# Kernel optimization log

Measured on AMD Instinct MI355X. Metric: run time of the kernel, lower is better.

Reference implementation:

```python
import jax, jax.numpy as jnp
import numpy as np

N_NODES = 100000
N_EDGES = 1600000
F_IN, F_HID, F_OUT = 15, 64, 64
N_MID = 6  # layers 1..6 of 8


def gcn_norm(edge_index, edge_weight, num_nodes):
    """PyG GCNConv normalization with self-loops (fill_value=1.0).
    Returns (src, dst, norm) over the augmented edge set."""
    src, dst = edge_index[0], edge_index[1]
    loop = jnp.arange(num_nodes)
    s = jnp.concatenate([src, loop])
    d = jnp.concatenate([dst, loop])
    w = jnp.concatenate([edge_weight, jnp.ones((num_nodes,), edge_weight.dtype)])
    deg = jax.ops.segment_sum(w, d, num_segments=num_nodes)
    dinv = jnp.where(deg > 0, jax.lax.rsqrt(deg), 0.0)
    norm = dinv[s] * w * dinv[d]  # [E+N]
    return s, d, norm


def gcn_layer(h, s, d, norm, W, b, num_nodes):
    h = h @ W                                  # dense transform [N, F_out]
    msg = norm[:, None] * h[s]                 # gather + scale   [E+N, F_out]
    out = jax.ops.segment_sum(msg, d, num_segments=num_nodes)  # scatter-add
    return out + b


def setup_inputs() -> dict:
    key = jax.random.key(0)
    ks = jax.random.split(key, 8)
    x = jax.random.normal(ks[0], (N_NODES, F_IN), jnp.float32)
    edge_index = jax.random.randint(ks[1], (2, N_EDGES), 0, N_NODES, jnp.int64)
    edge_weight = jax.random.uniform(ks[2], (N_EDGES,), jnp.float32)
    # glorot-ish scaling keeps activations sane through 8 layers
    W0 = jax.random.normal(ks[3], (F_IN, F_HID), jnp.float32) * (1.0 / np.sqrt(F_IN))
    b0 = jnp.zeros((F_HID,), jnp.float32)
    W_mid = jax.random.normal(ks[4], (N_MID, F_HID, F_HID), jnp.float32) * (1.0 / np.sqrt(F_HID))
    b_mid = jnp.zeros((N_MID, F_HID), jnp.float32)
    W_last = jax.random.normal(ks[5], (F_HID, F_OUT), jnp.float32) * (1.0 / np.sqrt(F_HID))
    b_last = jnp.zeros((F_OUT,), jnp.float32)
    return {"x": x, "edge_index": edge_index, "edge_weight": edge_weight,
            "W0": W0, "b0": b0, "W_mid": W_mid, "b_mid": b_mid,
            "W_last": W_last, "b_last": b_last}


def reference(x, edge_index, edge_weight, W0, b0, W_mid, b_mid, W_last, b_last):
    num_nodes = x.shape[0]
    s, d, norm = gcn_norm(edge_index, edge_weight, num_nodes)
    # layer 0
    h = gcn_layer(x, s, d, norm, W0, b0, num_nodes)
    h = jax.nn.relu(h)  # dropout is identity in eval mode
    # middle layers 1..6
    for i in range(N_MID):
        h = gcn_layer(h, s, d, norm, W_mid[i], b_mid[i], num_nodes)
        h = jax.nn.relu(h)
    # final layer + sigmoid
    h = gcn_layer(h, s, d, norm, W_last, b_last, num_nodes)
    return jax.nn.sigmoid(h)
```

## Files before the change

### kernel.cpp

```cpp
#include <hip/hip_runtime.h>
#include <hip/hip_fp16.h>
#include <math.h>

#define N_NODES 100000
#define N_EDGES 1600000
#define F_IN 15
#define MASK40 ((1ull << 40) - 1)

#define NBLK1 256
#define EPB   (N_EDGES / NBLK1)
#define NBUCK 256
#define NBUCK_USED ((N_NODES + 511) >> 9)

typedef _Float16 half8 __attribute__((ext_vector_type(8)));
typedef float f32x4 __attribute__((ext_vector_type(4)));


__global__ __launch_bounds__(1024) void k_hist(const int* __restrict__ dst,
                                               int* __restrict__ hist) {
    __shared__ int bins[NBUCK];
    int t = threadIdx.x, blk = blockIdx.x;
    if (t < NBUCK) bins[t] = 0;
    __syncthreads();
    int e0 = blk * EPB;
    for (int e = e0 + t; e < e0 + EPB; e += 1024)
        atomicAdd(&bins[dst[e] >> 9], 1);
    __syncthreads();
    if (t < NBUCK) hist[t * NBLK1 + blk] = bins[t];
}

__global__ __launch_bounds__(1024) void k_scan(int* __restrict__ hist,
                                               int* __restrict__ bucketBase,
                                               int* __restrict__ rowptr) {
    __shared__ int sc[1024];
    int t = threadIdx.x;
    int base = t * 64;
    int vals[64];
    int tot = 0;
#pragma unroll
    for (int k = 0; k < 64; k++) { vals[k] = hist[base + k]; tot += vals[k]; }
    sc[t] = tot;
    __syncthreads();
    for (int off = 1; off < 1024; off <<= 1) {
        int u = (t >= off) ? sc[t - off] : 0;
        __syncthreads();
        sc[t] += u;
        __syncthreads();
    }
    int run = sc[t] - tot;
#pragma unroll
    for (int k = 0; k < 64; k++) {
        int idx = base + k;
        if ((idx & (NBLK1 - 1)) == 0) bucketBase[idx / NBLK1] = run;
        int v = vals[k];
        hist[idx] = run;
        run += v;
    }
    if (t == 0) { bucketBase[NBUCK] = N_EDGES; rowptr[N_NODES] = N_EDGES; }
}

__global__ __launch_bounds__(1024) void k_scatter(const int* __restrict__ src,
        const int* __restrict__ dst, const float* __restrict__ w,
        const int* __restrict__ hist, int2* __restrict__ brec) {
    __shared__ int cursor[NBUCK];
    int t = threadIdx.x, blk = blockIdx.x;
    if (t < NBUCK) cursor[t] = hist[t * NBLK1 + blk];
    __syncthreads();
    int e0 = blk * EPB;
    for (int e = e0 + t; e < e0 + EPB; e += 1024) {
        int d = dst[e];
        int pos = atomicAdd(&cursor[d >> 9], 1);
        brec[pos] = make_int2(src[e] | ((d & 511) << 17), __float_as_int(w[e]));
    }
}

__global__ __launch_bounds__(512) void k_deg(const int2* __restrict__ brec,
        const int* __restrict__ bucketBase, float* __restrict__ dinv,
        int* __restrict__ rowptr) {
    __shared__ unsigned long long packedl[512];
    __shared__ int sc[512];
    int t = threadIdx.x, b = blockIdx.x;
    packedl[t] = 0ull;
    __syncthreads();
    int ebase = bucketBase[b], eend = bucketBase[b + 1];
    for (int e = ebase + t; e < eend; e += 512) {
        int2 r = brec[e];
        int dlo = (r.x >> 17) & 511;
        float wv = __int_as_float(r.y);
        unsigned long long contrib =
            (1ull << 40) + (unsigned long long)((double)wv * 4294967296.0);
        atomicAdd(&packedl[dlo], contrib);
    }
    __syncthreads();
    unsigned long long p = packedl[t];
    int cnt = (int)(p >> 40);
    int n = (b << 9) + t;
    if (n < N_NODES) {
        float deg = 1.0f + (float)((double)(p & MASK40) * 0x1p-32);
        dinv[n] = rsqrtf(deg);
    }
    sc[t] = cnt;
    __syncthreads();
    for (int off = 1; off < 512; off <<= 1) {
        int u = (t >= off) ? sc[t - off] : 0;
        __syncthreads();
        sc[t] += u;
        __syncthreads();
    }
    if (n < N_NODES) rowptr[n] = ebase + sc[t] - cnt;
}

__global__ __launch_bounds__(512) void k_csr(const int2* __restrict__ brec,
        const int* __restrict__ bucketBase, const int* __restrict__ rowptr,
        const float* __restrict__ dinv, int2* __restrict__ csr) {
    __shared__ int cursor[512];
    __shared__ float dl[512];
    int t = threadIdx.x, b = blockIdx.x;
    int n = (b << 9) + t;
    if (n < N_NODES) { cursor[t] = rowptr[n]; dl[t] = dinv[n]; }
    else             { cursor[t] = 0;         dl[t] = 0.f; }
    __syncthreads();
    int ebase = bucketBase[b], eend = bucketBase[b + 1];
    for (int e = ebase + t; e < eend; e += 512) {
        int2 r = brec[e];
        int dlo = (r.x >> 17) & 511;
        int s = r.x & 0x1FFFF;
        float wv = __int_as_float(r.y);
        int slot = atomicAdd(&cursor[dlo], 1);
        float nm = dinv[s] * wv * dl[dlo];
        csr[slot] = make_int2(s << 7, __float_as_int(nm));
    }
}


__global__ void k_gemm0(const float* __restrict__ x, const float* __restrict__ W,
                        __half* __restrict__ out) {
    __shared__ float Ws[F_IN * 64];
    int t = threadIdx.x;
    for (int i = t; i < F_IN * 64; i += 256) Ws[i] = W[i];
    __syncthreads();
    int r = blockIdx.x * 4 + (t >> 6);
    int c = t & 63;
    if (r < N_NODES) {
        const float* xr = x + r * F_IN;
        float acc = 0.f;
#pragma unroll
        for (int k = 0; k < F_IN; k++) acc += xr[k] * Ws[k * 64 + c];
        out[r * 64 + c] = __float2half(acc);
    }
}


#define SE_CAP 128
#define G_STRIDE 72

template <bool WEP, bool SIG>
__global__ __launch_bounds__(256, 8) void k_gather4(
        const int* __restrict__ rowptr, const int2* __restrict__ csr,
        const __half* __restrict__ hin, const float* __restrict__ dinv,
        const float* __restrict__ W, const float* __restrict__ b,
        void* __restrict__ outp) {
    extern __shared__ char smem[];
    int t = threadIdx.x, wv = t >> 6, lane = t & 63;
    int sub = lane >> 5, fl = lane & 31;
    int2* se = (int2*)smem + wv * SE_CAP;
    _Float16* G = (_Float16*)(smem + 4 * SE_CAP * 8);

    int nb = blockIdx.x * 32;
    int n0w = nb + wv * 8;

    int rp[9];
#pragma unroll
    for (int j = 0; j < 9; j++) rp[j] = rowptr[n0w + j];
    int base = rp[0], end = rp[8];

    const char* hb = (const char*)hin;
    unsigned flb = (unsigned)fl * 4u;

    const __half2* h2 = (const __half2*)hin;
    float2 acc[8];
#pragma unroll
    for (int j = 0; j < 8; j++) {
        int n = n0w + j;
        float dv = dinv[n];
        __half2 hq = h2[n * 32 + fl];
        float w0 = (sub == 0) ? dv * dv : 0.f;
        acc[j].x = w0 * __low2float(hq);
        acc[j].y = w0 * __high2float(hq);
    }

    for (int cb = base; cb < end; cb += SE_CAP) {
        int ce = cb + SE_CAP; if (ce > end) ce = end;
        int cn = ce - cb;
        for (int i = lane; i < cn; i += 64) se[i] = csr[cb + i];
        __builtin_amdgcn_wave_barrier();
#pragma unroll
        for (int j = 0; j < 8; j++) {
            int lo = rp[j] < cb ? cb : rp[j];
            int hi = rp[j + 1] > ce ? ce : rp[j + 1];
            int i = lo - cb, iend = hi - cb;
            for (; i + 7 < iend; i += 8) {
                int2 r0 = se[i + sub],     r1 = se[i + 2 + sub];
                int2 r2 = se[i + 4 + sub], r3 = se[i + 6 + sub];
                __half2 q0 = *(const __half2*)(hb + (size_t)((unsigned)r0.x + flb));
                __half2 q1 = *(const __half2*)(hb + (size_t)((unsigned)r1.x + flb));
                __half2 q2 = *(const __half2*)(hb + (size_t)((unsigned)r2.x + flb));
                __half2 q3 = *(const __half2*)(hb + (size_t)((unsigned)r3.x + flb));
                float n0 = __int_as_float(r0.y), n1 = __int_as_float(r1.y);
                float n2 = __int_as_float(r2.y), n3 = __int_as_float(r3.y);
                acc[j].x = fmaf(n0, __low2float(q0), acc[j].x);
                acc[j].y = fmaf(n0, __high2float(q0), acc[j].y);
                acc[j].x = fmaf(n1, __low2float(q1), acc[j].x);
                acc[j].y = fmaf(n1, __high2float(q1), acc[j].y);
                acc[j].x = fmaf(n2, __low2float(q2), acc[j].x);
                acc[j].y = fmaf(n2, __high2float(q2), acc[j].y);
                acc[j].x = fmaf(n3, __low2float(q3), acc[j].x);
                acc[j].y = fmaf(n3, __high2float(q3), acc[j].y);
            }
            for (; i + 1 < iend; i += 2) {
                int2 r = se[i + sub];
                __half2 q = *(const __half2*)(hb + (size_t)((unsigned)r.x + flb));
                float nm = __int_as_float(r.y);
                acc[j].x = fmaf(nm, __low2float(q), acc[j].x);
                acc[j].y = fmaf(nm, __high2float(q), acc[j].y);
            }
            if (i < iend) {
                int2 r = se[i];
                __half2 q = *(const __half2*)(hb + (size_t)((unsigned)r.x + flb));
                float nm = (sub == 0) ? __int_as_float(r.y) : 0.f;
                acc[j].x = fmaf(nm, __low2float(q), acc[j].x);
                acc[j].y = fmaf(nm, __high2float(q), acc[j].y);
            }
        }
        __builtin_amdgcn_wave_barrier();
    }

#pragma unroll
    for (int j = 0; j < 8; j++) {
        acc[j].x += __shfl_xor(acc[j].x, 32);
        acc[j].y += __shfl_xor(acc[j].y, 32);
    }

    if (!WEP) {
        float2 bv = ((const float2*)b)[fl];
        if (sub == 0) {
#pragma unroll
            for (int j = 0; j < 8; j++) {
                float ox = fmaxf(acc[j].x + bv.x, 0.f);
                float oy = fmaxf(acc[j].y + bv.y, 0.f);
                ((__half2*)outp)[(n0w + j) * 32 + fl] = __floats2half2_rn(ox, oy);
            }
        }
        return;
    }

    if (sub == 0) {
        __half2* G2 = (__half2*)G;
#pragma unroll
        for (int j = 0; j < 8; j++)
            G2[(wv * 8 + j) * (G_STRIDE / 2) + fl] = __floats2half2_rn(acc[j].x, acc[j].y);
    }
    __syncthreads();

    int col = lane & 15, quad = lane >> 4;
    int mrow = (wv & 1) * 16;
    int nc0 = (wv >> 1) * 32;

    half8 af[2];
#pragma unroll
    for (int kt = 0; kt < 2; kt++)
        af[kt] = *(const half8*)&G[(mrow + col) * G_STRIDE + kt * 32 + quad * 8];

    __syncthreads();

    half8 bf[2][2][2];
#pragma unroll
    for (int nt = 0; nt < 2; nt++) {
#pragma unroll
        for (int kt = 0; kt < 2; kt++) {
#pragma unroll
            for (int j = 0; j < 8; j++) {
                float w = W[(kt * 32 + quad * 8 + j) * 64 + nc0 + nt * 16 + col];
                _Float16 hi = (_Float16)w;
                bf[nt][kt][0][j] = hi;
                bf[nt][kt][1][j] = (_Float16)(w - (float)hi);
            }
        }
    }

    f32x4 c0, c1;
    {
        float b0v = b[nc0 + col], b1v = b[nc0 + 16 + col];
        c0 = (f32x4){b0v, b0v, b0v, b0v};
        c1 = (f32x4){b1v, b1v, b1v, b1v};
    }
#pragma unroll
    for (int kt = 0; kt < 2; kt++) {
        c0 = __builtin_amdgcn_mfma_f32_16x16x32_f16(af[kt], bf[0][kt][0], c0, 0, 0, 0);
        c0 = __builtin_amdgcn_mfma_f32_16x16x32_f16(af[kt], bf[0][kt][1], c0, 0, 0, 0);
        c1 = __builtin_amdgcn_mfma_f32_16x16x32_f16(af[kt], bf[1][kt][0], c1, 0, 0, 0);
        c1 = __builtin_amdgcn_mfma_f32_16x16x32_f16(af[kt], bf[1][kt][1], c1, 0, 0, 0);
    }

    if (!SIG) {
#pragma unroll
        for (int nt = 0; nt < 2; nt++) {
            f32x4 c = nt ? c1 : c0;
#pragma unroll
            for (int r = 0; r < 4; r++) {
                float o = fmaxf(c[r], 0.f);
                G[(mrow + quad * 4 + r) * G_STRIDE + nc0 + nt * 16 + col] =
                    (_Float16)o;
            }
        }
        __syncthreads();
        {
            int row = t >> 3, seg = t & 7;
            half8 v = *(const half8*)&G[row * G_STRIDE + seg * 8];
            *(half8*)((__half*)outp + (nb + row) * 64 + seg * 8) = v;
        }
    } else {
        float* fo = (float*)smem;
#pragma unroll
        for (int nt = 0; nt < 2; nt++) {
            f32x4 c = nt ? c1 : c0;
#pragma unroll
            for (int r = 0; r < 4; r++) {
                float o = 1.0f / (1.0f + expf(-c[r]));
                fo[(mrow + quad * 4 + r) * 66 + nc0 + nt * 16 + col] = o;
            }
        }
        __syncthreads();
#pragma unroll
        for (int k = 0; k < 2; k++) {
            int lin = t + k * 256;
            int row = lin >> 4, seg = lin & 15;
            float4 v = *(const float4*)&fo[row * 66 + seg * 4];
            *(float4*)((float*)outp + (nb + row) * 64 + seg * 4) = v;
        }
    }
}


extern "C" void kernel_launch(void* const* d_in, const int* in_sizes, int n_in,
                              void* d_out, int out_size, void* d_ws, size_t ws_size,
                              hipStream_t stream) {
    const float* x  = (const float*)d_in[0];
    const int*   ei = (const int*)  d_in[1];
    const float* ew = (const float*)d_in[2];
    const float* W0 = (const float*)d_in[3];
    const float* b0 = (const float*)d_in[4];
    const float* Wm = (const float*)d_in[5];
    const float* bm = (const float*)d_in[6];
    const float* Wl = (const float*)d_in[7];
    const float* bl = (const float*)d_in[8];
    float* out = (float*)d_out;

    const int* src = ei;
    const int* dst = ei + N_EDGES;

    char* ws = (char*)d_ws;
    int*    hist   = (int*)  (ws + 0);
    int*    bbase  = (int*)  (ws + (1u << 18));
    float*  dinv   = (float*)(ws + (1u << 20));
    int*    rowptr = (int*)  (ws + (2u << 20));
    int2*   brec   = (int2*) (ws + (3u << 20));
    int2*   csr    = (int2*) (ws + (16u << 20));
    __half* htmp   = (__half*)(ws + (29u << 20));
    __half* hA     = (__half*)(ws + (42u << 20));
    __half* hB     = (__half*)(ws + (55u << 20));

    int gR4 = (N_NODES + 3) / 4;
    int gG  = N_NODES / 32;

    const size_t smem0 = 4 * SE_CAP * 8;
    const size_t smemW = 4 * SE_CAP * 8 + 32 * G_STRIDE * 2;

    hipLaunchKernelGGL(k_hist,    dim3(NBLK1), dim3(1024), 0, stream, dst, hist);
    hipLaunchKernelGGL(k_scan,    dim3(1),     dim3(1024), 0, stream, hist, bbase, rowptr);
    hipLaunchKernelGGL(k_scatter, dim3(NBLK1), dim3(1024), 0, stream, src, dst, ew, hist, brec);
    hipLaunchKernelGGL(k_deg,     dim3(NBUCK_USED), dim3(512), 0, stream, brec, bbase, dinv, rowptr);
    hipLaunchKernelGGL(k_csr,     dim3(NBUCK_USED), dim3(512), 0, stream, brec, bbase, rowptr, dinv, csr);

    hipLaunchKernelGGL(k_gemm0,   dim3(gR4), dim3(256), 0, stream, x, W0, htmp);
    hipLaunchKernelGGL((k_gather4<false, false>), dim3(gG), dim3(256), smem0, stream,
                       rowptr, csr, htmp, dinv, (const float*)nullptr, b0, (void*)hA);

    __half* hin = hA;
    __half* hout = hB;
    for (int i = 0; i < 6; i++) {
        const float* Wi = Wm + (long)i * 64 * 64;
        const float* bi = bm + (long)i * 64;
        hipLaunchKernelGGL((k_gather4<true, false>), dim3(gG), dim3(256), smemW, stream,
                           rowptr, csr, hin, dinv, Wi, bi, (void*)hout);
        __half* t2 = hin; hin = hout; hout = t2;
    }

    hipLaunchKernelGGL((k_gather4<true, true>), dim3(gG), dim3(256), smemW, stream,
                       rowptr, csr, hin, dinv, Wl, bl, (void*)out);
}
```

Measured before the change: 506.0 us.

## Make gather kernels persistent with atomic tile queue for dynamic load balancing

The per-layer gather kernels now launch a fixed grid of 2048 blocks. Each block repeatedly takes the next 32-node tile from a global atomic counter until all 3125 tiles are done. The counters are zeroed in the scan kernel, one per layer. This aims to balance the uneven per-tile edge counts and cut block scheduling overhead, at the cost of an atomic and extra block-wide barriers per tile.

```diff
diff --git a/kernel.cpp b/kernel.cpp
--- a/kernel.cpp
+++ b/kernel.cpp
@@ -11,6 +11,9 @@
 #define EPB   (N_EDGES / NBLK1)
 #define NBUCK 256
 #define NBUCK_USED ((N_NODES + 511) >> 9)
+
+#define NT_TILES 3125
+#define PERSIST_BLOCKS 2048
 
 typedef _Float16 half8 __attribute__((ext_vector_type(8)));
 typedef float f32x4 __attribute__((ext_vector_type(4)));
@@ -31,7 +34,8 @@
 
 __global__ __launch_bounds__(1024) void k_scan(int* __restrict__ hist,
                                                int* __restrict__ bucketBase,
-                                               int* __restrict__ rowptr) {
+                                               int* __restrict__ rowptr,
+                                               int* __restrict__ tick) {
     __shared__ int sc[1024];
     int t = threadIdx.x;
     int base = t * 64;
@@ -57,6 +61,7 @@
         run += v;
     }
     if (t == 0) { bucketBase[NBUCK] = N_EDGES; rowptr[N_NODES] = N_EDGES; }
+    if (t < 8) tick[t] = 0;
 }
 
 __global__ __launch_bounds__(1024) void k_scatter(const int* __restrict__ src,
@@ -159,185 +164,195 @@
         const int* __restrict__ rowptr, const int2* __restrict__ csr,
         const __half* __restrict__ hin, const float* __restrict__ dinv,
         const float* __restrict__ W, const float* __restrict__ b,
-        void* __restrict__ outp) {
+        int* __restrict__ tick, void* __restrict__ outp) {
     extern __shared__ char smem[];
+    __shared__ int s_tile;
     int t = threadIdx.x, wv = t >> 6, lane = t & 63;
     int sub = lane >> 5, fl = lane & 31;
     int2* se = (int2*)smem + wv * SE_CAP;
     _Float16* G = (_Float16*)(smem + 4 * SE_CAP * 8);
 
-    int nb = blockIdx.x * 32;
-    int n0w = nb + wv * 8;
-
-    int rp[9];
-#pragma unroll
-    for (int j = 0; j < 9; j++) rp[j] = rowptr[n0w + j];
-    int base = rp[0], end = rp[8];
-
     const char* hb = (const char*)hin;
     unsigned flb = (unsigned)fl * 4u;
-
     const __half2* h2 = (const __half2*)hin;
-    float2 acc[8];
-#pragma unroll
-    for (int j = 0; j < 8; j++) {
-        int n = n0w + j;
-        float dv = dinv[n];
-        __half2 hq = h2[n * 32 + fl];
-        float w0 = (sub == 0) ? dv * dv : 0.f;
-        acc[j].x = w0 * __low2float(hq);
-        acc[j].y = w0 * __high2float(hq);
-    }
-
-    for (int cb = base; cb < end; cb += SE_CAP) {
-        int ce = cb + SE_CAP; if (ce > end) ce = end;
-        int cn = ce - cb;
-        for (int i = lane; i < cn; i += 64) se[i] = csr[cb + i];
-        __builtin_amdgcn_wave_barrier();
+
+    for (;;) {
+        if (t == 0) s_tile = atomicAdd(tick, 1);
+        __syncthreads();
+        int tile = s_tile;
+        if (tile >= NT_TILES) break;
+
+        int nb = tile * 32;
+        int n0w = nb + wv * 8;
+
+        int rp[9];
+#pragma unroll
+        for (int j = 0; j < 9; j++) rp[j] = rowptr[n0w + j];
+        int base = rp[0], end = rp[8];
+
+        float2 acc[8];
 #pragma unroll
         for (int j = 0; j < 8; j++) {
-            int lo = rp[j] < cb ? cb : rp[j];
-            int hi = rp[j + 1] > ce ? ce : rp[j + 1];
-            int i = lo - cb, iend = hi - cb;
-            for (; i + 7 < iend; i += 8) {
-                int2 r0 = se[i + sub],     r1 = se[i + 2 + sub];
-                int2 r2 = se[i + 4 + sub], r3 = se[i + 6 + sub];
-                __half2 q0 = *(const __half2*)(hb + (size_t)((unsigned)r0.x + flb));
-                __half2 q1 = *(const __half2*)(hb + (size_t)((unsigned)r1.x + flb));
-                __half2 q2 = *(const __half2*)(hb + (size_t)((unsigned)r2.x + flb));
-                __half2 q3 = *(const __half2*)(hb + (size_t)((unsigned)r3.x + flb));
-                float n0 = __int_as_float(r0.y), n1 = __int_as_float(r1.y);
-                float n2 = __int_as_float(r2.y), n3 = __int_as_float(r3.y);
-                acc[j].x = fmaf(n0, __low2float(q0), acc[j].x);
-                acc[j].y = fmaf(n0, __high2float(q0), acc[j].y);
-                acc[j].x = fmaf(n1, __low2float(q1), acc[j].x);
-                acc[j].y = fmaf(n1, __high2float(q1), acc[j].y);
-                acc[j].x = fmaf(n2, __low2float(q2), acc[j].x);
-                acc[j].y = fmaf(n2, __high2float(q2), acc[j].y);
-                acc[j].x = fmaf(n3, __low2float(q3), acc[j].x);
-                acc[j].y = fmaf(n3, __high2float(q3), acc[j].y);
-            }
-            for (; i + 1 < iend; i += 2) {
-                int2 r = se[i + sub];
-                __half2 q = *(const __half2*)(hb + (size_t)((unsigned)r.x + flb));
-                float nm = __int_as_float(r.y);
-                acc[j].x = fmaf(nm, __low2float(q), acc[j].x);
-                acc[j].y = fmaf(nm, __high2float(q), acc[j].y);
-            }
-            if (i < iend) {
-                int2 r = se[i];
-                __half2 q = *(const __half2*)(hb + (size_t)((unsigned)r.x + flb));
-                float nm = (sub == 0) ? __int_as_float(r.y) : 0.f;
-                acc[j].x = fmaf(nm, __low2float(q), acc[j].x);
-                acc[j].y = fmaf(nm, __high2float(q), acc[j].y);
-            }
-        }
-        __builtin_amdgcn_wave_barrier();
-    }
-
-#pragma unroll
-    for (int j = 0; j < 8; j++) {
-        acc[j].x += __shfl_xor(acc[j].x, 32);
-        acc[j].y += __shfl_xor(acc[j].y, 32);
-    }
-
-    if (!WEP) {
-        float2 bv = ((const float2*)b)[fl];
+            int n = n0w + j;
+            float dv = dinv[n];
+            __half2 hq = h2[n * 32 + fl];
+            float w0 = (sub == 0) ? dv * dv : 0.f;
+            acc[j].x = w0 * __low2float(hq);
+            acc[j].y = w0 * __high2float(hq);
+        }
+
+        for (int cb = base; cb < end; cb += SE_CAP) {
+            int ce = cb + SE_CAP; if (ce > end) ce = end;
+            int cn = ce - cb;
+            for (int i = lane; i < cn; i += 64) se[i] = csr[cb + i];
+            __builtin_amdgcn_wave_barrier();
+#pragma unroll
+            for (int j = 0; j < 8; j++) {
+                int lo = rp[j] < cb ? cb : rp[j];
+                int hi = rp[j + 1] > ce ? ce : rp[j + 1];
+                int i = lo - cb, iend = hi - cb;
+                for (; i + 7 < iend; i += 8) {
+                    int2 r0 = se[i + sub],     r1 = se[i + 2 + sub];
+                    int2 r2 = se[i + 4 + sub], r3 = se[i + 6 + sub];
+                    __half2 q0 = *(const __half2*)(hb + (size_t)((unsigned)r0.x + flb));
+                    __half2 q1 = *(const __half2*)(hb + (size_t)((unsigned)r1.x + flb));
+                    __half2 q2 = *(const __half2*)(hb + (size_t)((unsigned)r2.x + flb));
+                    __half2 q3 = *(const __half2*)(hb + (size_t)((unsigned)r3.x + flb));
+                    float n0 = __int_as_float(r0.y), n1 = __int_as_float(r1.y);
+                    float n2 = __int_as_float(r2.y), n3 = __int_as_float(r3.y);
+                    acc[j].x = fmaf(n0, __low2float(q0), acc[j].x);
+                    acc[j].y = fmaf(n0, __high2float(q0), acc[j].y);
+                    acc[j].x = fmaf(n1, __low2float(q1), acc[j].x);
+                    acc[j].y = fmaf(n1, __high2float(q1), acc[j].y);
+                    acc[j].x = fmaf(n2, __low2float(q2), acc[j].x);
+                    acc[j].y = fmaf(n2, __high2float(q2), acc[j].y);
+                    acc[j].x = fmaf(n3, __low2float(q3), acc[j].x);
+                    acc[j].y = fmaf(n3, __high2float(q3), acc[j].y);
+                }
+                for (; i + 1 < iend; i += 2) {
+                    int2 r = se[i + sub];
+                    __half2 q = *(const __half2*)(hb + (size_t)((unsigned)r.x + flb));
+                    float nm = __int_as_float(r.y);
+                    acc[j].x = fmaf(nm, __low2float(q), acc[j].x);
+                    acc[j].y = fmaf(nm, __high2float(q), acc[j].y);
+                }
+                if (i < iend) {
+                    int2 r = se[i];
+                    __half2 q = *(const __half2*)(hb + (size_t)((unsigned)r.x + flb));
+                    float nm = (sub == 0) ? __int_as_float(r.y) : 0.f;
+                    acc[j].x = fmaf(nm, __low2float(q), acc[j].x);
+                    acc[j].y = fmaf(nm, __high2float(q), acc[j].y);
+                }
+            }
+            __builtin_amdgcn_wave_barrier();
+        }
+
+#pragma unroll
+        for (int j = 0; j < 8; j++) {
+            acc[j].x += __shfl_xor(acc[j].x, 32);
+            acc[j].y += __shfl_xor(acc[j].y, 32);
+        }
+
+        if (!WEP) {
+            float2 bv = ((const float2*)b)[fl];
+            if (sub == 0) {
+#pragma unroll
+                for (int j = 0; j < 8; j++) {
+                    float ox = fmaxf(acc[j].x + bv.x, 0.f);
+                    float oy = fmaxf(acc[j].y + bv.y, 0.f);
+                    ((__half2*)outp)[(n0w + j) * 32 + fl] = __floats2half2_rn(ox, oy);
+                }
+            }
+            __syncthreads();
+            continue;
+        }
+
         if (sub == 0) {
-#pragma unroll
-            for (int j = 0; j < 8; j++) {
-                float ox = fmaxf(acc[j].x + bv.x, 0.f);
-                float oy = fmaxf(acc[j].y + bv.y, 0.f);
-                ((__half2*)outp)[(n0w + j) * 32 + fl] = __floats2half2_rn(ox, oy);
-            }
-        }
-        return;
-    }
-
-    if (sub == 0) {
-        __half2* G2 = (__half2*)G;
-#pragma unroll
-        for (int j = 0; j < 8; j++)
-            G2[(wv * 8 + j) * (G_STRIDE / 2) + fl] = __floats2half2_rn(acc[j].x, acc[j].y);
-    }
-    __syncthreads();
-
-    int col = lane & 15, quad = lane >> 4;
-    int mrow = (wv & 1) * 16;
-    int nc0 = (wv >> 1) * 32;
-
-    half8 af[2];
-#pragma unroll
-    for (int kt = 0; kt < 2; kt++)
-        af[kt] = *(const half8*)&G[(mrow + col) * G_STRIDE + kt * 32 + quad * 8];
-
-    __syncthreads();
-
-    half8 bf[2][2][2];
-#pragma unroll
-    for (int nt = 0; nt < 2; nt++) {
+            __half2* G2 = (__half2*)G;
+#pragma unroll
+            for (int j = 0; j < 8; j++)
+                G2[(wv * 8 + j) * (G_STRIDE / 2) + fl] = __floats2half2_rn(acc[j].x, acc[j].y);
+        }
+        __syncthreads();
+
+        int col = lane & 15, quad = lane >> 4;
+        int mrow = (wv & 1) * 16;
+        int nc0 = (wv >> 1) * 32;
+
+        half8 af[2];
+#pragma unroll
+        for (int kt = 0; kt < 2; kt++)
+            af[kt] = *(const half8*)&G[(mrow + col) * G_STRIDE + kt * 32 + quad * 8];
+
+        __syncthreads();
+
+        half8 bf[2][2][2];
+#pragma unroll
+        for (int nt = 0; nt < 2; nt++) {
+#pragma unroll
+            for (int kt = 0; kt < 2; kt++) {
+#pragma unroll
+                for (int j = 0; j < 8; j++) {
+                    float w = W[(kt * 32 + quad * 8 + j) * 64 + nc0 + nt * 16 + col];
+                    _Float16 hi = (_Float16)w;
+                    bf[nt][kt][0][j] = hi;
+                    bf[nt][kt][1][j] = (_Float16)(w - (float)hi);
+                }
+            }
+        }
+
+        f32x4 c0, c1;
+        {
+            float b0v = b[nc0 + col], b1v = b[nc0 + 16 + col];
+            c0 = (f32x4){b0v, b0v, b0v, b0v};
+            c1 = (f32x4){b1v, b1v, b1v, b1v};
+        }
 #pragma unroll
         for (int kt = 0; kt < 2; kt++) {
-#pragma unroll
-            for (int j = 0; j < 8; j++) {
-                float w = W[(kt * 32 + quad * 8 + j) * 64 + nc0 + nt * 16 + col];
-                _Float16 hi = (_Float16)w;
-                bf[nt][kt][0][j] = hi;
-                bf[nt][kt][1][j] = (_Float16)(w - (float)hi);
-            }
-        }
-    }
-
-    f32x4 c0, c1;
-    {
-        float b0v = b[nc0 + col], b1v = b[nc0 + 16 + col];
-        c0 = (f32x4){b0v, b0v, b0v, b0v};
-        c1 = (f32x4){b1v, b1v, b1v, b1v};
-    }
-#pragma unroll
-    for (int kt = 0; kt < 2; kt++) {
-        c0 = __builtin_amdgcn_mfma_f32_16x16x32_f16(af[kt], bf[0][kt][0], c0, 0, 0, 0);
-        c0 = __builtin_amdgcn_mfma_f32_16x16x32_f16(af[kt], bf[0][kt][1], c0, 0, 0, 0);
-        c1 = __builtin_amdgcn_mfma_f32_16x16x32_f16(af[kt], bf[1][kt][0], c1, 0, 0, 0);
-        c1 = __builtin_amdgcn_mfma_f32_16x16x32_f16(af[kt], bf[1][kt][1], c1, 0, 0, 0);
-    }
-
-    if (!SIG) {
-#pragma unroll
-        for (int nt = 0; nt < 2; nt++) {
-            f32x4 c = nt ? c1 : c0;
-#pragma unroll
-            for (int r = 0; r < 4; r++) {
-                float o = fmaxf(c[r], 0.f);
-                G[(mrow + quad * 4 + r) * G_STRIDE + nc0 + nt * 16 + col] =
-                    (_Float16)o;
-            }
-        }
-        __syncthreads();
-        {
-            int row = t >> 3, seg = t & 7;
-            half8 v = *(const half8*)&G[row * G_STRIDE + seg * 8];
-            *(half8*)((__half*)outp + (nb + row) * 64 + seg * 8) = v;
-        }
-    } else {
-        float* fo = (float*)smem;
-#pragma unroll
-        for (int nt = 0; nt < 2; nt++) {
-            f32x4 c = nt ? c1 : c0;
-#pragma unroll
-            for (int r = 0; r < 4; r++) {
-                float o = 1.0f / (1.0f + expf(-c[r]));
-                fo[(mrow + quad * 4 + r) * 66 + nc0 + nt * 16 + col] = o;
-            }
-        }
-        __syncthreads();
-#pragma unroll
-        for (int k = 0; k < 2; k++) {
-            int lin = t + k * 256;
-            int row = lin >> 4, seg = lin & 15;
-            float4 v = *(const float4*)&fo[row * 66 + seg * 4];
-            *(float4*)((float*)outp + (nb + row) * 64 + seg * 4) = v;
-        }
+            c0 = __builtin_amdgcn_mfma_f32_16x16x32_f16(af[kt], bf[0][kt][0], c0, 0, 0, 0);
+            c0 = __builtin_amdgcn_mfma_f32_16x16x32_f16(af[kt], bf[0][kt][1], c0, 0, 0, 0);
+            c1 = __builtin_amdgcn_mfma_f32_16x16x32_f16(af[kt], bf[1][kt][0], c1, 0, 0, 0);
+            c1 = __builtin_amdgcn_mfma_f32_16x16x32_f16(af[kt], bf[1][kt][1], c1, 0, 0, 0);
+        }
+
+        if (!SIG) {
+#pragma unroll
+            for (int nt = 0; nt < 2; nt++) {
+                f32x4 c = nt ? c1 : c0;
+#pragma unroll
+                for (int r = 0; r < 4; r++) {
+                    float o = fmaxf(c[r], 0.f);
+                    G[(mrow + quad * 4 + r) * G_STRIDE + nc0 + nt * 16 + col] =
+                        (_Float16)o;
+                }
+            }
+            __syncthreads();
+            {
+                int row = t >> 3, seg = t & 7;
+                half8 v = *(const half8*)&G[row * G_STRIDE + seg * 8];
+                *(half8*)((__half*)outp + (nb + row) * 64 + seg * 8) = v;
+            }
+        } else {
+            float* fo = (float*)smem;
+#pragma unroll
+            for (int nt = 0; nt < 2; nt++) {
+                f32x4 c = nt ? c1 : c0;
+#pragma unroll
+                for (int r = 0; r < 4; r++) {
+                    float o = 1.0f / (1.0f + expf(-c[r]));
+                    fo[(mrow + quad * 4 + r) * 66 + nc0 + nt * 16 + col] = o;
+                }
+            }
+            __syncthreads();
+#pragma unroll
+            for (int k = 0; k < 2; k++) {
+                int lin = t + k * 256;
+                int row = lin >> 4, seg = lin & 15;
+                float4 v = *(const float4*)&fo[row * 66 + seg * 4];
+                *(float4*)((float*)outp + (nb + row) * 64 + seg * 4) = v;
+            }
+        }
+        __syncthreads();
     }
 }
 
@@ -362,6 +377,7 @@
     char* ws = (char*)d_ws;
     int*    hist   = (int*)  (ws + 0);
     int*    bbase  = (int*)  (ws + (1u << 18));
+    int*    tick   = (int*)  (ws + (1u << 18) + 8192);
     float*  dinv   = (float*)(ws + (1u << 20));
     int*    rowptr = (int*)  (ws + (2u << 20));
     int2*   brec   = (int2*) (ws + (3u << 20));
@@ -371,31 +387,30 @@
     __half* hB     = (__half*)(ws + (55u << 20));
 
     int gR4 = (N_NODES + 3) / 4;
-    int gG  = N_NODES / 32;
 
     const size_t smem0 = 4 * SE_CAP * 8;
     const size_t smemW = 4 * SE_CAP * 8 + 32 * G_STRIDE * 2;
 
     hipLaunchKernelGGL(k_hist,    dim3(NBLK1), dim3(1024), 0, stream, dst, hist);
-    hipLaunchKernelGGL(k_scan,    dim3(1),     dim3(1024), 0, stream, hist, bbase, rowptr);
+    hipLaunchKernelGGL(k_scan,    dim3(1),     dim3(1024), 0, stream, hist, bbase, rowptr, tick);
     hipLaunchKernelGGL(k_scatter, dim3(NBLK1), dim3(1024), 0, stream, src, dst, ew, hist, brec);
     hipLaunchKernelGGL(k_deg,     dim3(NBUCK_USED), dim3(512), 0, stream, brec, bbase, dinv, rowptr);
     hipLaunchKernelGGL(k_csr,     dim3(NBUCK_USED), dim3(512), 0, stream, brec, bbase, rowptr, dinv, csr);
 
     hipLaunchKernelGGL(k_gemm0,   dim3(gR4), dim3(256), 0, stream, x, W0, htmp);
-    hipLaunchKernelGGL((k_gather4<false, false>), dim3(gG), dim3(256), smem0, stream,
-                       rowptr, csr, htmp, dinv, (const float*)nullptr, b0, (void*)hA);
+    hipLaunchKernelGGL((k_gather4<false, false>), dim3(PERSIST_BLOCKS), dim3(256), smem0, stream,
+                       rowptr, csr, htmp, dinv, (const float*)nullptr, b0, tick + 0, (void*)hA);
 
     __half* hin = hA;
     __half* hout = hB;
     for (int i = 0; i < 6; i++) {
         const float* Wi = Wm + (long)i * 64 * 64;
         const float* bi = bm + (long)i * 64;
-        hipLaunchKernelGGL((k_gather4<true, false>), dim3(gG), dim3(256), smemW, stream,
-                           rowptr, csr, hin, dinv, Wi, bi, (void*)hout);
+        hipLaunchKernelGGL((k_gather4<true, false>), dim3(PERSIST_BLOCKS), dim3(256), smemW, stream,
+                           rowptr, csr, hin, dinv, Wi, bi, tick + 1 + i, (void*)hout);
         __half* t2 = hin; hin = hout; hout = t2;
     }
 
-    hipLaunchKernelGGL((k_gather4<true, true>), dim3(gG), dim3(256), smemW, stream,
-                       rowptr, csr, hin, dinv, Wl, bl, (void*)out);
-}
+    hipLaunchKernelGGL((k_gather4<true, true>), dim3(PERSIST_BLOCKS), dim3(256), smemW, stream,
+                       rowptr, csr, hin, dinv, Wl, bl, tick + 7, (void*)out);
+}
```

Result: slower. 1.260 ms (+149.0%).
